# Performance work log

Measured on AMD Instinct MI355X. Metric: run time of the kernel, lower is better.

## Reference

```python
import jax, jax.numpy as jnp
import numpy as np

STRIDE = 16
SCALES = (8, 16, 32)
RATIOS = (0.5, 1.0, 2.0)
PRE_NMS_TOPN = 6000
POST_NMS_TOPN = 300
NMS_THRESH = 0.7
MIN_SIZE = 16.0


def _mkanchors(ws, hs, xc, yc):
    ws = ws[:, None]; hs = hs[:, None]
    return np.hstack([xc - 0.5 * (ws - 1), yc - 0.5 * (hs - 1),
                      xc + 0.5 * (ws - 1), yc + 0.5 * (hs - 1)])


def _base_anchors():
    base = np.array([0.0, 0.0, STRIDE - 1.0, STRIDE - 1.0])
    w = base[2] - base[0] + 1; h = base[3] - base[1] + 1
    xc = base[0] + 0.5 * (w - 1); yc = base[1] + 0.5 * (h - 1)
    size = w * h
    ratios = np.array(RATIOS)
    ws = np.round(np.sqrt(size / ratios)); hs = np.round(ws * ratios)
    ra = _mkanchors(ws, hs, xc, yc)  # [3,4]
    out = []
    for a in ra:
        aw = a[2] - a[0] + 1; ah = a[3] - a[1] + 1
        axc = a[0] + 0.5 * (aw - 1); ayc = a[1] + 0.5 * (ah - 1)
        s = np.array(SCALES)
        out.append(_mkanchors(aw * s, ah * s, axc, ayc))
    return np.vstack(out).astype(np.float32)  # [9,4]


def _all_anchors(H, W):
    base = _base_anchors()  # [A,4]
    sx = np.arange(W) * STRIDE; sy = np.arange(H) * STRIDE
    gx, gy = np.meshgrid(sx, sy)  # [H,W]
    shifts = np.stack([gx.ravel(), gy.ravel(), gx.ravel(), gy.ravel()], axis=1)
    return (shifts[:, None, :].astype(np.float32) + base[None, :, :]).reshape(-1, 4)


def conv2d(x, w, b, pad):
    y = jax.lax.conv_general_dilated(x, w, (1, 1), [(pad, pad), (pad, pad)],
                                     dimension_numbers=('NCHW', 'OIHW', 'NCHW'))
    return y + b[None, :, None, None]


def rpn_forward(feature_map, im_info, conv_w, conv_b, cls_w, cls_b, bbox_w, bbox_b):
    x = jax.nn.relu(conv2d(feature_map, conv_w, conv_b, 1))
    cls_score = conv2d(x, cls_w, cls_b, 0)   # [1, 2A, H, W]
    bbox_pred = conv2d(x, bbox_w, bbox_b, 0)  # [1, 4A, H, W]
    b, c, H, W = cls_score.shape
    A = c // 2
    # softmax over (bg, fg) pairs: view(b,2,A,H,W), softmax dim=1
    prob = jax.nn.softmax(cls_score.reshape(b, 2, A, H, W), axis=1).reshape(b, c, H, W)
    scores = prob[0, A:].transpose(1, 2, 0).reshape(-1)       # fg scores [H*W*A]
    deltas = bbox_pred[0].transpose(1, 2, 0).reshape(-1, 4)   # [H*W*A, 4]
    anchors = jnp.asarray(_all_anchors(H, W))

    # bbox_transform_inv
    aw = anchors[:, 2] - anchors[:, 0] + 1.0
    ah = anchors[:, 3] - anchors[:, 1] + 1.0
    acx = anchors[:, 0] + 0.5 * aw
    acy = anchors[:, 1] + 0.5 * ah
    cx = deltas[:, 0] * aw + acx
    cy = deltas[:, 1] * ah + acy
    pw = jnp.exp(deltas[:, 2]) * aw
    ph = jnp.exp(deltas[:, 3]) * ah
    # clip to image
    x1 = jnp.clip(cx - 0.5 * pw, 0.0, im_info[1] - 1.0)
    y1 = jnp.clip(cy - 0.5 * ph, 0.0, im_info[0] - 1.0)
    x2 = jnp.clip(cx + 0.5 * pw, 0.0, im_info[1] - 1.0)
    y2 = jnp.clip(cy + 0.5 * ph, 0.0, im_info[0] - 1.0)
    boxes = jnp.stack([x1, y1, x2, y2], axis=1)

    # min-size filter (mask via -inf scores to keep shapes static)
    ms = MIN_SIZE * im_info[2]
    keep = ((x2 - x1 + 1.0) >= ms) & ((y2 - y1 + 1.0) >= ms)
    scores = jnp.where(keep, scores, -jnp.inf)

    # pre-NMS top-k (sorted descending)
    sc, idx = jax.lax.top_k(scores, PRE_NMS_TOPN)
    bx = boxes[idx]  # [P,4]
    areas = (bx[:, 2] - bx[:, 0] + 1.0) * (bx[:, 3] - bx[:, 1] + 1.0)

    def nms_step(supp, _):
        avail = jnp.where(supp, -jnp.inf, sc)
        i = jnp.argmax(avail)
        valid = avail[i] > -jnp.inf
        box = bx[i]
        xx1 = jnp.maximum(box[0], bx[:, 0]); yy1 = jnp.maximum(box[1], bx[:, 1])
        xx2 = jnp.minimum(box[2], bx[:, 2]); yy2 = jnp.minimum(box[3], bx[:, 3])
        inter = jnp.maximum(xx2 - xx1 + 1.0, 0.0) * jnp.maximum(yy2 - yy1 + 1.0, 0.0)
        iou = inter / (areas[i] + areas - inter)
        supp = supp | (iou > NMS_THRESH)  # suppresses i itself (iou==1)
        out_box = jnp.where(valid, box, jnp.zeros((4,), box.dtype))
        return supp, out_box

    supp0 = jnp.zeros((PRE_NMS_TOPN,), dtype=bool)
    _, kept = jax.lax.scan(nms_step, supp0, None, length=POST_NMS_TOPN)  # [300,4]
    rois = jnp.concatenate([jnp.zeros((POST_NMS_TOPN, 1), kept.dtype), kept], axis=1)
    return rois  # [300, 5] (batch_idx, x1, y1, x2, y2)


def setup_inputs() -> dict:
    key = jax.random.key(0)
    ks = jax.random.split(key, 7)
    C, A = 512, 9
    H, W = 64, 96  # feature map for a 1024x1536 image at stride 16
    std = 0.01  # weight_init gaussian std in the repo
    return {
        'feature_map': jax.random.normal(ks[0], (1, C, H, W), jnp.float32),
        'im_info': jnp.array([1024.0, 1536.0, 1.0], jnp.float32),
        'conv_w': std * jax.random.normal(ks[1], (C, C, 3, 3), jnp.float32),
        'conv_b': jnp.zeros((C,), jnp.float32),
        'cls_w': std * jax.random.normal(ks[2], (2 * A, C, 1, 1), jnp.float32),
        'cls_b': jnp.zeros((2 * A,), jnp.float32),
        'bbox_w': std * jax.random.normal(ks[3], (4 * A, C, 1, 1), jnp.float32),
        'bbox_b': jnp.zeros((4 * A,), jnp.float32),
    }


def reference(feature_map, im_info, conv_w, conv_b, cls_w, cls_b, bbox_w, bbox_b):
    return rpn_forward(feature_map, im_info, conv_w, conv_b, cls_w, cls_b, bbox_w, bbox_b)
```

## Files before the change

### kernel.cpp

```cpp
#include <hip/hip_runtime.h>
#include <stdint.h>

typedef unsigned int u32;
typedef unsigned long long u64;
typedef __attribute__((ext_vector_type(8))) short v8s;
typedef __attribute__((ext_vector_type(4))) float v4f;

#define HH 64
#define WW 96
#define HW 6144
#define CC 512
#define NANCH 55296
#define PRE 6000
#define POST 300
#define CAP 8192
#define PW 98
#define PH 66
#define ICPAD 40
#define NHB 384

__device__ __constant__ float c_aw[9] = {184.f,368.f,736.f,128.f,256.f,512.f,88.f,176.f,352.f};
__device__ __constant__ float c_ah[9] = {96.f,192.f,384.f,128.f,256.f,512.f,176.f,352.f,704.f};

__device__ __forceinline__ unsigned short bf16_rne(float x){
  u32 u = __float_as_uint(x);
  return (unsigned short)((u + 0x7FFFu + ((u >> 16) & 1u)) >> 16);
}
__device__ __forceinline__ u32 sortkey(float s){
  u32 u = __float_as_uint(s);
  return u ^ ((u & 0x80000000u) ? 0xFFFFFFFFu : 0x80000000u);
}

__global__ __launch_bounds__(256) void k_cvt(const float* __restrict__ X, const float* __restrict__ Wt,
                                             const float* __restrict__ cw, const float* __restrict__ bw,
                                             unsigned short* __restrict__ Xih, unsigned short* __restrict__ Xil,
                                             unsigned short* __restrict__ Wh2, unsigned short* __restrict__ Wl2,
                                             float* __restrict__ Whd, u32* __restrict__ zero_region){
  __shared__ float Ls[64][97];
  __shared__ float Ws[4608];
  const int b = blockIdx.x, tid = threadIdx.x;
  { int gid = b*256 + tid;
    if (gid < 163856) zero_region[gid] = 0u; }
  if (b < 528){
    const int rp  = b % 66;
    const int ic0 = (b / 66) * 64;
    const bool zrow = (rp == 0 || rp == PH-1);
    if (!zrow){
      int r = rp - 1;
      for (int i = tid; i < 6144; i += 256){
        int ii = i / 96, c = i - ii*96;
        Ls[ii][c] = X[(ic0+ii)*HW + r*WW + c];
      }
    }
    __syncthreads();
    for (int idx = tid; idx < 98*16; idx += 256){
      int cp = idx >> 4, g = idx & 15;
      int icl0 = g*4;
      u64 hv = 0, lv = 0;
      #pragma unroll
      for (int u = 0; u < 4; ++u){
        float x = 0.f;
        if (!zrow && cp >= 1 && cp <= 96) x = Ls[icl0+u][cp-1];
        unsigned short h = bf16_rne(x);
        float hf = __uint_as_float(((u32)h) << 16);
        unsigned short l = bf16_rne(x - hf);
        hv |= ((u64)h) << (16*u);
        lv |= ((u64)l) << (16*u);
      }
      long o = ((long)(rp*PW + cp) << 9) + ic0 + icl0;
      *reinterpret_cast<u64*>(Xih + o) = hv;
      *reinterpret_cast<u64*>(Xil + o) = lv;
    }
  } else if (b < 1040){
    const int oc = b - 528;
    for (int i = tid; i < 4608; i += 256) Ws[i] = Wt[oc*4608 + i];
    __syncthreads();
    for (int idx = tid; idx < 9*128; idx += 256){
      int tap = idx >> 7, g = idx & 127;
      int icb = g*4;
      u64 hv = 0, lv = 0;
      #pragma unroll
      for (int u = 0; u < 4; ++u){
        float x = Ws[(icb+u)*9 + tap];
        unsigned short h = bf16_rne(x);
        float hf = __uint_as_float(((u32)h) << 16);
        unsigned short l = bf16_rne(x - hf);
        hv |= ((u64)h) << (16*u);
        lv |= ((u64)l) << (16*u);
      }
      long o = ((long)(tap*512 + oc) << 9) + icb;
      *reinterpret_cast<u64*>(Wh2 + o) = hv;
      *reinterpret_cast<u64*>(Wl2 + o) = lv;
    }
  } else {
    int idx = (b - 1040)*256 + tid;
    int o  = idx >> 9;
    int gc = idx & 511;
    float v = 0.f;
    if (o < 18) v = cw[o*512 + gc];
    else if (o < 54) v = bw[(o-18)*512 + gc];
    Whd[gc*64 + o] = v;
  }
}

__global__ __launch_bounds__(256, 1) void k_conv3(
    const unsigned short* __restrict__ Xih, const unsigned short* __restrict__ Xil,
    const unsigned short* __restrict__ Wh2, const unsigned short* __restrict__ Wl2,
    const float* __restrict__ Bc, float* __restrict__ Y)
{
  __shared__ __attribute__((aligned(16))) unsigned short Ah[6*98*ICPAD];
  __shared__ __attribute__((aligned(16))) unsigned short Al[6*98*ICPAD];
  __shared__ __attribute__((aligned(16))) unsigned short Bh[9*32*ICPAD];
  __shared__ __attribute__((aligned(16))) unsigned short Bl[9*32*ICPAD];
  const int tid  = threadIdx.x;
  const int w    = tid >> 6;
  const int lane = tid & 63;
  const int lm   = lane & 15;
  const int q    = lane >> 4;
  const int y0   = blockIdx.x * 4;
  const int oc0  = blockIdx.y * 32;

  v4f acc[6][2];
  #pragma unroll
  for (int t = 0; t < 6; ++t)
    #pragma unroll
    for (int n = 0; n < 2; ++n)
      acc[t][n] = (v4f){0.f,0.f,0.f,0.f};

  u64 ra[19][2], rb[9][2];
  auto loadSlab = [&](int icg){
    #pragma unroll
    for (int n = 0; n < 19; ++n){
      int it = tid + 256*n;
      if (it < 4704){
        int i4 = it & 7, rc = it >> 3;
        int c = rc % 98, r = rc / 98;
        long src = ((long)((y0 + r)*PW + c) << 9) + icg*32 + i4*4;
        ra[n][0] = *reinterpret_cast<const u64*>(Xih + src);
        ra[n][1] = *reinterpret_cast<const u64*>(Xil + src);
      }
    }
    #pragma unroll
    for (int n = 0; n < 9; ++n){
      int it = tid + 256*n;
      if (it < 2304){
        int i4 = it & 7, to = it >> 3;
        int oc = to & 31, tap = to >> 5;
        long src = ((long)(tap*512 + oc0 + oc) << 9) + icg*32 + i4*4;
        rb[n][0] = *reinterpret_cast<const u64*>(Wh2 + src);
        rb[n][1] = *reinterpret_cast<const u64*>(Wl2 + src);
      }
    }
  };
  auto storeSlab = [&](){
    #pragma unroll
    for (int n = 0; n < 19; ++n){
      int it = tid + 256*n;
      if (it < 4704){
        int i4 = it & 7, rc = it >> 3;
        int dst = rc*ICPAD + i4*4;
        *reinterpret_cast<u64*>(Ah + dst) = ra[n][0];
        *reinterpret_cast<u64*>(Al + dst) = ra[n][1];
      }
    }
    #pragma unroll
    for (int n = 0; n < 9; ++n){
      int it = tid + 256*n;
      if (it < 2304){
        int i4 = it & 7, to = it >> 3;
        int dst = to*ICPAD + i4*4;
        *reinterpret_cast<u64*>(Bh + dst) = rb[n][0];
        *reinterpret_cast<u64*>(Bl + dst) = rb[n][1];
      }
    }
  };

  loadSlab(0);
  for (int icg = 0; icg < 16; ++icg){
    __syncthreads();
    storeSlab();
    __syncthreads();
    if (icg < 15) loadSlab(icg + 1);
    #pragma unroll
    for (int tap = 0; tap < 9; ++tap){
      const int dy = tap / 3, dx = tap - dy*3;
      v8s ah[6], al[6], bh[2], bl[2];
      #pragma unroll
      for (int t = 0; t < 6; ++t){
        int a = ((w + dy)*98 + 16*t + lm + dx)*ICPAD + q*8;
        ah[t] = *reinterpret_cast<const v8s*>(Ah + a);
        al[t] = *reinterpret_cast<const v8s*>(Al + a);
      }
      #pragma unroll
      for (int n = 0; n < 2; ++n){
        int a = (tap*32 + n*16 + lm)*ICPAD + q*8;
        bh[n] = *reinterpret_cast<const v8s*>(Bh + a);
        bl[n] = *reinterpret_cast<const v8s*>(Bl + a);
      }
      #pragma unroll
      for (int t = 0; t < 6; ++t)
        #pragma unroll
        for (int n = 0; n < 2; ++n){
          acc[t][n] = __builtin_amdgcn_mfma_f32_16x16x32_bf16(al[t], bl[n], acc[t][n], 0, 0, 0);
          acc[t][n] = __builtin_amdgcn_mfma_f32_16x16x32_bf16(al[t], bh[n], acc[t][n], 0, 0, 0);
          acc[t][n] = __builtin_amdgcn_mfma_f32_16x16x32_bf16(ah[t], bl[n], acc[t][n], 0, 0, 0);
          acc[t][n] = __builtin_amdgcn_mfma_f32_16x16x32_bf16(ah[t], bh[n], acc[t][n], 0, 0, 0);
        }
    }
  }
  const int yrow = y0 + w;
  #pragma unroll
  for (int n = 0; n < 2; ++n){
    int oc = oc0 + n*16 + lm;
    float b = Bc[oc];
    #pragma unroll
    for (int t = 0; t < 6; ++t){
      float4 v;
      v.x = fmaxf(acc[t][n].x + b, 0.f);
      v.y = fmaxf(acc[t][n].y + b, 0.f);
      v.z = fmaxf(acc[t][n].z + b, 0.f);
      v.w = fmaxf(acc[t][n].w + b, 0.f);
      *reinterpret_cast<float4*>(Y + (long)oc*HW + yrow*WW + 16*t + q*4) = v;
    }
  }
}

__global__ __launch_bounds__(256) void k_head(
    const float* __restrict__ Y, const float* __restrict__ Whd,
    const float* __restrict__ cb, const float* __restrict__ bb,
    const float* __restrict__ info,
    float* __restrict__ scores, float4* __restrict__ boxes, u32* __restrict__ hist8g)
{
  __shared__ float Ys[1024];
  __shared__ float Wsh[4096];
  __shared__ u32 lh[256];
  const int tid = threadIdx.x;
  const int p0  = blockIdx.x * 16;
  const int po  = tid & 15;
  const int oj  = tid >> 4;
  lh[tid] = 0u;
  float accM[4], accC[4];
  #pragma unroll
  for (int k = 0; k < 4; ++k){ accM[k] = 0.f; accC[k] = 0.f; }

  for (int c0 = 0; c0 < CC; c0 += 64){
    __syncthreads();
    for (int i = tid; i < 1024; i += 256){
      int c = i >> 4, p = i & 15;
      Ys[i] = Y[(c0 + c) * HW + p0 + p];
    }
    for (int i = tid; i < 4096; i += 256){
      int c = i >> 6, o = i & 63;
      Wsh[c*64 + (o & 15)*4 + (o >> 4)] = Whd[(c0 + c)*64 + o];
    }
    __syncthreads();
    #pragma unroll 4
    for (int c = 0; c < 64; ++c){
      float xa = Ys[c*16 + po];
      float4 wv = *reinterpret_cast<const float4*>(Wsh + c*64 + oj*4);
      accC[0] = __fmaf_rn(xa, wv.x, accC[0]);
      accC[1] = __fmaf_rn(xa, wv.y, accC[1]);
      accC[2] = __fmaf_rn(xa, wv.z, accC[2]);
      accC[3] = __fmaf_rn(xa, wv.w, accC[3]);
    }
    #pragma unroll
    for (int k = 0; k < 4; ++k){ accM[k] += accC[k]; accC[k] = 0.f; }
  }
  __syncthreads();
  #pragma unroll
  for (int k = 0; k < 4; ++k){
    int o = oj + 16*k;
    float bias = (o < 18) ? cb[o] : ((o < 54) ? bb[o - 18] : 0.f);
    Ys[po*64 + o] = accM[k] + bias;
  }
  __syncthreads();
  float imH = info[0], imW = info[1], imS = info[2];
  for (int it = tid; it < 144; it += 256){
    int pl = it / 9;
    int a  = it - pl*9;
    const float* L = Ys + pl*64;
    float l0 = L[a], l1 = L[9 + a];
    float mx = fmaxf(l0, l1);
    float e0 = expf(l0 - mx), e1 = expf(l1 - mx);
    float sc = e1 / (e0 + e1);
    float d0 = L[18 + a*4 + 0], d1 = L[18 + a*4 + 1];
    float d2 = L[18 + a*4 + 2], d3 = L[18 + a*4 + 3];
    int pos = p0 + pl;
    int yy = pos / 96;
    int xx = pos - yy * 96;
    float aw = c_aw[a], ah = c_ah[a];
    float acx = (float)(xx * 16 + 8);
    float acy = (float)(yy * 16 + 8);
    float cx = __fadd_rn(__fmul_rn(d0, aw), acx);
    float cy = __fadd_rn(__fmul_rn(d1, ah), acy);
    float pw = __fmul_rn(expf(d2), aw);
    float ph = __fmul_rn(expf(d3), ah);
    float hx = __fmul_rn(0.5f, pw);
    float hy = __fmul_rn(0.5f, ph);
    float x1 = fminf(fmaxf(__fadd_rn(cx, -hx), 0.f), imW - 1.f);
    float y1 = fminf(fmaxf(__fadd_rn(cy, -hy), 0.f), imH - 1.f);
    float x2 = fminf(fmaxf(__fadd_rn(cx,  hx), 0.f), imW - 1.f);
    float y2 = fminf(fmaxf(__fadd_rn(cy,  hy), 0.f), imH - 1.f);
    float ms = 16.f * imS;
    bool keep = ((x2 - x1 + 1.f) >= ms) && ((y2 - y1 + 1.f) >= ms);
    int g = pos * 9 + a;
    float val = keep ? sc : -__builtin_inff();
    scores[g] = val;
    boxes[g]  = make_float4(x1, y1, x2, y2);
    atomicAdd(&lh[sortkey(val) >> 24], 1u);
  }
  __syncthreads();
  hist8g[blockIdx.x*256 + tid] = lh[tid];
}

__global__ __launch_bounds__(1024) void k_sel(const u32* __restrict__ hist8g, u32* __restrict__ hist2,
                                              const float* __restrict__ scores,
                                              u32* __restrict__ ctr, u64* __restrict__ keys){
  __shared__ u32 cs[1024];
  __shared__ u32 bs[64];
  __shared__ u32 h8[256];
  __shared__ u32 lh2[256];
  __shared__ int selg;
  __shared__ u32 afterv, T16s, aboves, K32s, B8s, above8s;
  const int t = threadIdx.x;
  const int b0 = t * 64;

  { int g = t >> 8, bin = t & 255;
    u32 s = 0;
    for (int b = g; b < NHB; b += 4) s += hist8g[b*256 + bin];
    cs[t] = s; }
  __syncthreads();
  if (t < 256){
    h8[t] = cs[t] + cs[256 + t] + cs[512 + t] + cs[768 + t];
    lh2[t] = 0u;
  }
  __syncthreads();
  if (t == 0){
    u32 acc = 0;
    for (int bin = 255; bin >= 0; --bin){
      acc += h8[bin];
      if (acc >= 6000u){ B8s = (u32)bin; above8s = acc - h8[bin]; break; }
    }
  }
  __syncthreads();

  { u32 b8 = B8s;
    const float4* s4 = reinterpret_cast<const float4*>(scores);
    for (int i = t; i < NANCH/4; i += 1024){
      float4 v = s4[i];
      u32 k0 = sortkey(v.x), k1 = sortkey(v.y), k2 = sortkey(v.z), k3 = sortkey(v.w);
      if ((k0 >> 24) == b8) atomicAdd(&lh2[(k0 >> 16) & 0xFFu], 1u);
      if ((k1 >> 24) == b8) atomicAdd(&lh2[(k1 >> 16) & 0xFFu], 1u);
      if ((k2 >> 24) == b8) atomicAdd(&lh2[(k2 >> 16) & 0xFFu], 1u);
      if ((k3 >> 24) == b8) atomicAdd(&lh2[(k3 >> 16) & 0xFFu], 1u);
    } }
  __syncthreads();
  if (t == 0){
    u32 acc = above8s;
    for (int bin = 255; bin >= 0; --bin){
      acc += lh2[bin];
      if (acc >= 6000u){ T16s = (B8s << 8) | (u32)bin; aboves = acc - lh2[bin]; break; }
    }
  }
  __syncthreads();

  { u32 pfx = T16s;
    const float4* s4 = reinterpret_cast<const float4*>(scores);
    for (int i = t; i < NANCH/4; i += 1024){
      float4 v = s4[i];
      u32 k0 = sortkey(v.x), k1 = sortkey(v.y), k2 = sortkey(v.z), k3 = sortkey(v.w);
      if ((k0 >> 16) == pfx) atomicAdd(&hist2[k0 & 0xFFFFu], 1u);
      if ((k1 >> 16) == pfx) atomicAdd(&hist2[k1 & 0xFFFFu], 1u);
      if ((k2 >> 16) == pfx) atomicAdd(&hist2[k2 & 0xFFFFu], 1u);
      if ((k3 >> 16) == pfx) atomicAdd(&hist2[k3 & 0xFFFFu], 1u);
    } }
  __threadfence();
  __syncthreads();

  if (t == 0) selg = -1;
  __syncthreads();
  const u32 target = 6000u - aboves;
  { u32 s = 0;
    for (int i = 0; i < 64; ++i) s += hist2[b0 + i];
    cs[t] = s; }
  __syncthreads();
  for (int off = 1; off < 1024; off <<= 1){
    u32 v = cs[t];
    u32 ad = (t + off < 1024) ? cs[t + off] : 0u;
    __syncthreads();
    cs[t] = v + ad;
    __syncthreads();
  }
  { u32 here  = cs[t];
    u32 after = (t < 1023) ? cs[t + 1] : 0u;
    if (here >= target && after < target){ selg = t; afterv = after; } }
  __syncthreads();
  { int g = selg;
    if (g >= 0 && t < 64) bs[t] = hist2[g*64 + t];
    __syncthreads();
    if (t == 0){
      if (g < 0) K32s = (T16s << 16);
      else {
        u32 acc = afterv;
        for (int b = 63; b >= 0; --b){
          u32 h = bs[b];
          acc += h;
          if (acc >= target){ K32s = (T16s << 16) | (u32)(g*64 + b); break; }
        }
      }
      ctr[4] = 6000u;
    } }
  __syncthreads();

  { u32 K = K32s;
    const int lane = t & 63;
    const float4* s4 = reinterpret_cast<const float4*>(scores);
    for (int i = t; i < NANCH/4; i += 1024){
      float4 v = s4[i];
      u32 kk[4] = {sortkey(v.x), sortkey(v.y), sortkey(v.z), sortkey(v.w)};
      u64 m[4];
      #pragma unroll
      for (int u = 0; u < 4; ++u) m[u] = __ballot(kk[u] >= K);
      u32 tot = (u32)(__popcll(m[0]) + __popcll(m[1]) + __popcll(m[2]) + __popcll(m[3]));
      if (tot){
        u32 base = 0;
        if (lane == 0) base = atomicAdd(&ctr[0], tot);
        base = (u32)__shfl((int)base, 0, 64);
        u64 below = ((u64)1 << lane) - 1;
        u32 off = 0;
        #pragma unroll
        for (int u = 0; u < 4; ++u){
          if (kk[u] >= K){
            u32 pos = base + off + (u32)__popcll(m[u] & below);
            if (pos < CAP) keys[pos] = ((u64)kk[u] << 32) | (u64)(u32)(~(u32)(i*4 + u));
          }
          off += (u32)__popcll(m[u]);
        }
      }
    } }
}

__global__ __launch_bounds__(512) void k_rank(const u64* __restrict__ keys, u32* __restrict__ ctr,
                                              const float4* __restrict__ boxes,
                                              float4* __restrict__ topB, float* __restrict__ topA){
  __shared__ u64 ks[CAP];
  __shared__ u32 part[8][64];
  const int t  = threadIdx.x;
  const int s  = t >> 6;
  const int k  = t & 63;
  const int gi = blockIdx.x * 64 + k;
  u32 count = ctr[0]; if (count > CAP) count = CAP;
  u64 my = (gi < (int)count) ? keys[gi] : 0ull;
  for (int j = t; j < CAP; j += 512)
    ks[j] = (j < (int)count) ? keys[j] : 0ull;
  __syncthreads();
  int rank = 0;
  { const ulonglong2* kp = reinterpret_cast<const ulonglong2*>(ks + s*1024);
    #pragma unroll 8
    for (int j = 0; j < 512; ++j){
      ulonglong2 kv = kp[j];
      rank += (kv.x > my) + (kv.y > my);
    } }
  part[s][k] = (u32)rank;
  __syncthreads();
  if (t < 64){
    int r = 0;
    #pragma unroll
    for (int ss = 0; ss < 8; ++ss) r += part[ss][k];
    bool sel = (gi < (int)count && r < PRE);
    int myv = 0x7FFFFFFF;
    if (sel && !((my >> 32) & 0x80000000ull)) myv = r;
    #pragma unroll
    for (int off = 32; off; off >>= 1){
      int o = __shfl_down(myv, off, 64);
      myv = (o < myv) ? o : myv;
    }
    if (k == 0 && myv != 0x7FFFFFFF) atomicMin((int*)(ctr + 4), myv);
    if (sel){
      u32 idx = ~(u32)my;
      float4 bv = make_float4(0.f,0.f,0.f,0.f);
      float area = 1.f;
      if (idx < NANCH){
        bv = boxes[idx];
        area = (bv.z - bv.x + 1.f) * (bv.w - bv.y + 1.f);
      }
      topB[r] = bv;
      topA[r] = area;
    }
  }
}

__global__ __launch_bounds__(256) void k_nms3(const float4* __restrict__ topB,
                                              const u32* __restrict__ ctr, float* __restrict__ out){
  __shared__ float4 kb[POST];
  __shared__ float4 bx2[64];
  __shared__ u64    am[4];
  __shared__ int    nkS;
  const int tid  = threadIdx.x;
  const int wv   = tid >> 6;
  const int lane = tid & 63;
  int validN = (int)ctr[0];
  int finN   = (int)ctr[4];
  if (finN < validN) validN = finN;
  if (validN > PRE)  validN = PRE;
  if (tid == 0) nkS = 0;
  __syncthreads();

  float4 bnx = make_float4(0.f,0.f,0.f,0.f);
  if (lane < validN) bnx = topB[lane];

  for (int base = 0; base < validN; base += 64){
    int nk = nkS;
    if (nk >= POST) break;
    int c = base + lane;
    bool alive = (c < validN);
    float4 b = bnx;
    float ar = alive ? (b.z - b.x + 1.f) * (b.w - b.y + 1.f) : 1.f;
    if (wv == 0) bx2[lane] = b;
    { int cn = base + 64 + lane;
      if (cn < validN) bnx = topB[cn]; }
    int j = wv;
    for (; j + 28 < nk; j += 32){
      float4 kx[8];
      #pragma unroll
      for (int u = 0; u < 8; ++u) kx[u] = kb[j + 4*u];
      #pragma unroll
      for (int u = 0; u < 8; ++u){
        float kar = (kx[u].z - kx[u].x + 1.f) * (kx[u].w - kx[u].y + 1.f);
        float xx1 = fmaxf(kx[u].x, b.x);
        float yy1 = fmaxf(kx[u].y, b.y);
        float xx2 = fminf(kx[u].z, b.z);
        float yy2 = fminf(kx[u].w, b.w);
        float iw = fmaxf(xx2 - xx1 + 1.f, 0.f);
        float ih = fmaxf(yy2 - yy1 + 1.f, 0.f);
        float inter = iw * ih;
        float iou = inter / (kar + ar - inter);
        if (iou > 0.7f) alive = false;
      }
    }
    for (; j < nk; j += 4){
      float4 kbx = kb[j];
      float kar = (kbx.z - kbx.x + 1.f) * (kbx.w - kbx.y + 1.f);
      float xx1 = fmaxf(kbx.x, b.x);
      float yy1 = fmaxf(kbx.y, b.y);
      float xx2 = fminf(kbx.z, b.z);
      float yy2 = fminf(kbx.w, b.w);
      float iw = fmaxf(xx2 - xx1 + 1.f, 0.f);
      float ih = fmaxf(yy2 - yy1 + 1.f, 0.f);
      float inter = iw * ih;
      float iou = inter / (kar + ar - inter);
      if (iou > 0.7f) alive = false;
    }
    { u64 bal = __ballot(alive);
      if (lane == 0) am[wv] = bal; }
    __syncthreads();
    if (wv == 0){
      u64 comb = am[0] & am[1] & am[2] & am[3];
      alive = ((comb >> lane) & 1ull) != 0ull;
      int nkl = nk;
      while (nkl < POST){
        u64 bal = __ballot(alive);
        if (!bal) break;
        int L = (int)__ffsll((unsigned long long)bal) - 1;
        float4 pb = bx2[L];
        float pa = (pb.z - pb.x + 1.f) * (pb.w - pb.y + 1.f);
        if (lane == 0) kb[nkl] = pb;
        nkl++;
        if (lane == L) alive = false;
        if (alive){
          float xx1 = fmaxf(pb.x, b.x);
          float yy1 = fmaxf(pb.y, b.y);
          float xx2 = fminf(pb.z, b.z);
          float yy2 = fminf(pb.w, b.w);
          float iw = fmaxf(xx2 - xx1 + 1.f, 0.f);
          float ih = fmaxf(yy2 - yy1 + 1.f, 0.f);
          float inter = iw * ih;
          float iou = inter / (pa + ar - inter);
          if (iou > 0.7f) alive = false;
        }
      }
      if (lane == 0) nkS = nkl;
    }
    __syncthreads();
  }
  int nk = nkS;
  for (int q = tid; q < 1500; q += 256){
    int r = q / 5, c = q - r*5;
    float v = 0.f;
    if (r < nk && c > 0){
      float4 bx = kb[r];
      v = (c == 1) ? bx.x : (c == 2) ? bx.y : (c == 3) ? bx.z : bx.w;
    }
    out[q] = v;
  }
}

extern "C" void kernel_launch(void* const* d_in, const int* in_sizes, int n_in,
                              void* d_out, int out_size, void* d_ws, size_t ws_size,
                              hipStream_t stream)
{
  const float* fm   = (const float*)d_in[0];
  const float* info = (const float*)d_in[1];
  const float* cw3  = (const float*)d_in[2];
  const float* cb3  = (const float*)d_in[3];
  const float* clw  = (const float*)d_in[4];
  const float* clb  = (const float*)d_in[5];
  const float* bbw  = (const float*)d_in[6];
  const float* bbb  = (const float*)d_in[7];
  float* out = (float*)d_out;

  char* base = (char*)d_ws;
  u32*   hist8g = (u32*)  (base + 0);
  u32*   hist2  = (u32*)  (base + 393216);
  u32*   ctr    = (u32*)  (base + 655360);
  float* Y      = (float*)(base + 655424);
  float* scores = (float*)(base + 13238336);
  float4* boxes = (float4*)(base + 13459520);
  u64*   keys   = (u64*)  (base + 14344256);
  float4* topB  = (float4*)(base + 14409792);
  float* topA   = (float*)(base + 14505792);
  unsigned short* Xih = (unsigned short*)(base + 14529792);
  unsigned short* Xil = (unsigned short*)(base + 21153024);
  unsigned short* Wh2 = (unsigned short*)(base + 27776256);
  unsigned short* Wl2 = (unsigned short*)(base + 32494848);
  float* Whd = (float*)(base + 37213440);

  k_cvt   <<<1168, 256, 0, stream>>>(fm, cw3, clw, bbw, Xih, Xil, Wh2, Wl2, Whd, (u32*)base);
  k_conv3 <<<dim3(16, 16), 256, 0, stream>>>(Xih, Xil, Wh2, Wl2, cb3, Y);
  k_head  <<<384, 256, 0, stream>>>(Y, Whd, clb, bbb, info, scores, boxes, hist8g);
  k_sel   <<<1,  1024, 0, stream>>>(hist8g, hist2, scores, ctr, keys);
  k_rank  <<<128, 512, 0, stream>>>(keys, ctr, boxes, topB, topA);
  k_nms3  <<<1,   256, 0, stream>>>(topB, ctr, out);
}
```

Before: 409.2 us.

## Prefetch head tiles into registers, wave-shuffle scan in select, widen rank grid

The head kernel now loads the next channel chunk of Y and weights into registers while the current chunk is being computed, hiding global load latency behind the FMA loop. The select kernel replaces a 10-step shared-memory Hillis-Steele scan, which had many barriers, with a wave-level shuffle scan plus a small cross-wave scan. The rank kernel processes 32 keys per block over 16 slices instead of 64 over 8, doubling the grid to 256 blocks for more parallelism. The trade-offs are higher register pressure in the head kernel and each rank block re-loading the full key array into shared memory.

Result: faster. 359.2 us (-12.2%).

```diff
diff --git a/kernel.cpp b/kernel.cpp
--- a/kernel.cpp
+++ b/kernel.cpp
@@ -243,17 +243,39 @@
   #pragma unroll
   for (int k = 0; k < 4; ++k){ accM[k] = 0.f; accC[k] = 0.f; }
 
+  float yreg[4], wreg[16];
+  auto preload = [&](int c0){
+    #pragma unroll
+    for (int u = 0; u < 4; ++u){
+      int i = tid + 256*u;
+      yreg[u] = Y[(c0 + (i >> 4))*HW + p0 + (i & 15)];
+    }
+    #pragma unroll
+    for (int u = 0; u < 16; ++u){
+      int i = tid + 256*u;
+      wreg[u] = Whd[(c0 + (i >> 6))*64 + (i & 63)];
+    }
+  };
+  auto stash = [&](){
+    #pragma unroll
+    for (int u = 0; u < 4; ++u){
+      int i = tid + 256*u;
+      Ys[i] = yreg[u];
+    }
+    #pragma unroll
+    for (int u = 0; u < 16; ++u){
+      int i = tid + 256*u;
+      int c = i >> 6, o = i & 63;
+      Wsh[c*64 + (o & 15)*4 + (o >> 4)] = wreg[u];
+    }
+  };
+
+  preload(0);
   for (int c0 = 0; c0 < CC; c0 += 64){
     __syncthreads();
-    for (int i = tid; i < 1024; i += 256){
-      int c = i >> 4, p = i & 15;
-      Ys[i] = Y[(c0 + c) * HW + p0 + p];
-    }
-    for (int i = tid; i < 4096; i += 256){
-      int c = i >> 6, o = i & 63;
-      Wsh[c*64 + (o & 15)*4 + (o >> 4)] = Whd[(c0 + c)*64 + o];
-    }
-    __syncthreads();
+    stash();
+    __syncthreads();
+    if (c0 + 64 < CC) preload(c0 + 64);
     #pragma unroll 4
     for (int c = 0; c < 64; ++c){
       float xa = Ys[c*16 + po];
@@ -320,9 +342,12 @@
   __shared__ u32 bs[64];
   __shared__ u32 h8[256];
   __shared__ u32 lh2[256];
+  __shared__ u32 wsum[16], wsfx[16];
   __shared__ int selg;
   __shared__ u32 afterv, T16s, aboves, K32s, B8s, above8s;
   const int t = threadIdx.x;
+  const int lane = t & 63;
+  const int wv   = t >> 6;
   const int b0 = t * 64;
 
   { int g = t >> 8, bin = t & 255;
@@ -382,13 +407,26 @@
   const u32 target = 6000u - aboves;
   { u32 s = 0;
     for (int i = 0; i < 64; ++i) s += hist2[b0 + i];
-    cs[t] = s; }
-  __syncthreads();
-  for (int off = 1; off < 1024; off <<= 1){
-    u32 v = cs[t];
-    u32 ad = (t + off < 1024) ? cs[t + off] : 0u;
-    __syncthreads();
-    cs[t] = v + ad;
+    u32 v = s;
+    #pragma unroll
+    for (int off = 1; off < 64; off <<= 1){
+      u32 o = (u32)__shfl((int)v, lane + off, 64);
+      if (lane + off < 64) v += o;
+    }
+    if (lane == 0) wsum[wv] = v;
+    __syncthreads();
+    if (t < 16){
+      u32 x = wsum[t];
+      u32 vv = x;
+      #pragma unroll
+      for (int off = 1; off < 16; off <<= 1){
+        u32 o = (u32)__shfl((int)vv, t + off, 64);
+        if (t + off < 16) vv += o;
+      }
+      wsfx[t] = vv - x;
+    }
+    __syncthreads();
+    cs[t] = v + wsfx[wv];
     __syncthreads();
   }
   { u32 here  = cs[t];
@@ -413,7 +451,6 @@
   __syncthreads();
 
   { u32 K = K32s;
-    const int lane = t & 63;
     const float4* s4 = reinterpret_cast<const float4*>(scores);
     for (int i = t; i < NANCH/4; i += 1024){
       float4 v = s4[i];
@@ -444,49 +481,51 @@
                                               const float4* __restrict__ boxes,
                                               float4* __restrict__ topB, float* __restrict__ topA){
   __shared__ u64 ks[CAP];
-  __shared__ u32 part[8][64];
+  __shared__ u32 part[16][32];
   const int t  = threadIdx.x;
-  const int s  = t >> 6;
-  const int k  = t & 63;
-  const int gi = blockIdx.x * 64 + k;
+  const int s  = t >> 5;
+  const int k  = t & 31;
+  const int gi = blockIdx.x * 32 + k;
   u32 count = ctr[0]; if (count > CAP) count = CAP;
   u64 my = (gi < (int)count) ? keys[gi] : 0ull;
   for (int j = t; j < CAP; j += 512)
     ks[j] = (j < (int)count) ? keys[j] : 0ull;
   __syncthreads();
   int rank = 0;
-  { const ulonglong2* kp = reinterpret_cast<const ulonglong2*>(ks + s*1024);
+  { const ulonglong2* kp = reinterpret_cast<const ulonglong2*>(ks + s*512);
     #pragma unroll 8
-    for (int j = 0; j < 512; ++j){
+    for (int j = 0; j < 256; ++j){
       ulonglong2 kv = kp[j];
       rank += (kv.x > my) + (kv.y > my);
     } }
   part[s][k] = (u32)rank;
   __syncthreads();
+  int r = 0;
+  if (t < 32){
+    #pragma unroll
+    for (int ss = 0; ss < 16; ++ss) r += part[ss][k];
+  }
+  bool sel = (t < 32) && (gi < (int)count) && (r < PRE);
+  int myv = 0x7FFFFFFF;
+  if (sel && !((my >> 32) & 0x80000000ull)) myv = r;
   if (t < 64){
-    int r = 0;
-    #pragma unroll
-    for (int ss = 0; ss < 8; ++ss) r += part[ss][k];
-    bool sel = (gi < (int)count && r < PRE);
-    int myv = 0x7FFFFFFF;
-    if (sel && !((my >> 32) & 0x80000000ull)) myv = r;
     #pragma unroll
     for (int off = 32; off; off >>= 1){
       int o = __shfl_down(myv, off, 64);
       myv = (o < myv) ? o : myv;
     }
-    if (k == 0 && myv != 0x7FFFFFFF) atomicMin((int*)(ctr + 4), myv);
-    if (sel){
-      u32 idx = ~(u32)my;
-      float4 bv = make_float4(0.f,0.f,0.f,0.f);
-      float area = 1.f;
-      if (idx < NANCH){
-        bv = boxes[idx];
-        area = (bv.z - bv.x + 1.f) * (bv.w - bv.y + 1.f);
-      }
-      topB[r] = bv;
-      topA[r] = area;
-    }
+    if (t == 0 && myv != 0x7FFFFFFF) atomicMin((int*)(ctr + 4), myv);
+  }
+  if (sel){
+    u32 idx = ~(u32)my;
+    float4 bv = make_float4(0.f,0.f,0.f,0.f);
+    float area = 1.f;
+    if (idx < NANCH){
+      bv = boxes[idx];
+      area = (bv.z - bv.x + 1.f) * (bv.w - bv.y + 1.f);
+    }
+    topB[r] = bv;
+    topA[r] = area;
   }
 }
 
@@ -629,6 +668,6 @@
   k_conv3 <<<dim3(16, 16), 256, 0, stream>>>(Xih, Xil, Wh2, Wl2, cb3, Y);
   k_head  <<<384, 256, 0, stream>>>(Y, Whd, clb, bbb, info, scores, boxes, hist8g);
   k_sel   <<<1,  1024, 0, stream>>>(hist8g, hist2, scores, ctr, keys);
-  k_rank  <<<128, 512, 0, stream>>>(keys, ctr, boxes, topB, topA);
+  k_rank  <<<256, 512, 0, stream>>>(keys, ctr, boxes, topB, topA);
   k_nms3  <<<1,   256, 0, stream>>>(topB, ctr, out);
 }
```
